# Kernel tuning notes

Measured on AMD Instinct MI355X. Metric: run time of the kernel, lower is better.

The kernel has to match this reference:

```python
import jax, jax.numpy as jnp
import numpy as np

HIDDEN = 512
HEADS = 8
NORM = 1.0 / np.sqrt(HIDDEN // HEADS)  # torch: 1/sqrt(tensor(dim_k)//head) = 1/8


def setup_inputs() -> dict:
    key = jax.random.key(0)
    ks = jax.random.split(key, 14)
    B, N, D = 2, 2048, HIDDEN
    s = 0.02
    d = {
        "x_re": jax.random.normal(ks[0], (B, N, D), dtype=jnp.float32),
        "x_im": jax.random.normal(ks[1], (B, N, D), dtype=jnp.float32),
    }
    names = ["Wq_re", "Wq_im", "bq_re", "bq_im",
             "Wk_re", "Wk_im", "bk_re", "bk_im",
             "Wv_re", "Wv_im", "bv_re", "bv_im"]
    for i, nm in enumerate(names):
        shape = (D, D) if nm.startswith("W") else (D,)
        d[nm] = jax.random.normal(ks[2 + i], shape, dtype=jnp.float32) * s
    return d


def reference(x_re, x_im,
              Wq_re, Wq_im, bq_re, bq_im,
              Wk_re, Wk_im, bk_re, bk_im,
              Wv_re, Wv_im, bv_re, bv_im):
    B, N, D = x_re.shape
    h, dk = HEADS, D // HEADS
    x = jax.lax.complex(x_re, x_im)
    Wq = jax.lax.complex(Wq_re, Wq_im); bq = jax.lax.complex(bq_re, bq_im)
    Wk = jax.lax.complex(Wk_re, Wk_im); bk = jax.lax.complex(bk_re, bk_im)
    Wv = jax.lax.complex(Wv_re, Wv_im); bv = jax.lax.complex(bv_re, bv_im)

    def proj(W, b):  # torch nn.Linear: x @ W.T + b, then split heads -> [B,h,N,dk]
        y = x @ W.T + b
        return y.reshape(B, N, h, dk).transpose(0, 2, 1, 3)

    q, k, v = proj(Wq, bq), proj(Wk, bk), proj(Wv, bv)
    # complex matmul (no conjugation, matching torch.matmul), scaled
    dist = jnp.einsum("bhnd,bhmd->bhnm", q, k) * NORM
    probs = jax.nn.softmax(jnp.abs(dist), axis=-1).astype(jnp.complex64)
    att = jnp.einsum("bhnm,bhmd->bhnd", probs, v)
    att = att.transpose(0, 2, 1, 3).reshape(B, N, D)
    # real-view output [B, N, D, 2]
    return jnp.stack([att.real, att.imag], axis=-1)
```

## Files before the change

### kernel.cpp

```cpp
#include <hip/hip_runtime.h>
#include <hip/hip_bf16.h>
#include <math.h>

#define B_ 2
#define N_ 2048
#define D_ 512
#define H_ 8
#define DK_ 64
#define M_ (B_ * N_)

typedef short s16x8 __attribute__((ext_vector_type(8)));
typedef short s16x4 __attribute__((ext_vector_type(4)));
typedef float fx4   __attribute__((ext_vector_type(4)));
typedef int   ix4   __attribute__((ext_vector_type(4)));

static __device__ __forceinline__ short f2bf(float f) {
    __hip_bfloat16 h = __float2bfloat16(f);
    return __builtin_bit_cast(short, h);
}
static __device__ __forceinline__ float bf2f(short s) {
    unsigned int u = ((unsigned int)(unsigned short)s) << 16;
    return __builtin_bit_cast(float, u);
}
static __device__ __forceinline__ float fexp2(float x) {
#if __has_builtin(__builtin_amdgcn_exp2f)
    return __builtin_amdgcn_exp2f(x);
#else
    return exp2f(x);
#endif
}
static __device__ __forceinline__ float fsqrt_(float x) {
#if __has_builtin(__builtin_amdgcn_sqrtf)
    return __builtin_amdgcn_sqrtf(x);
#else
    return sqrtf(x);
#endif
}
static __device__ __forceinline__ int pack_tr(float a, float b) {
    unsigned ua = __builtin_bit_cast(unsigned, a);
    unsigned ub = __builtin_bit_cast(unsigned, b);
    return (int)((ua >> 16) | (ub & 0xFFFF0000u));
}

#define MFMA16(a, b, c) __builtin_amdgcn_mfma_f32_16x16x32_bf16(a, b, c, 0, 0, 0)

#define C2_ 0.18033688f
#define M0_ 16.0f

__global__ __launch_bounds__(256, 2)
void qkproj_mfma(const float* __restrict__ xr, const float* __restrict__ xi,
                 const float* __restrict__ W0r, const float* __restrict__ W0i,
                 const float* __restrict__ b0r, const float* __restrict__ b0i,
                 const float* __restrict__ W1r, const float* __restrict__ W1i,
                 const float* __restrict__ b1r, const float* __restrict__ b1i,
                 short* __restrict__ o0r, short* __restrict__ o0i,
                 short* __restrict__ o1r, short* __restrict__ o1i)
{
    __shared__ short sA[2][128][40];
    __shared__ short sB[2][64][40];

    const int tid = threadIdx.x;
    const int w = tid >> 6, l = tid & 63, lg = l >> 4, lc = l & 15;
    const int wr = w >> 1, wc = w & 1;
    const int bn = blockIdx.x, bm = blockIdx.y, z = blockIdx.z;
    const float* Wr = z ? W1r : W0r;
    const float* Wi = z ? W1i : W0i;
    const float* br = z ? b1r : b0r;
    const float* bi = z ? b1i : b0i;
    short* outr = z ? o1r : o0r;
    short* outi = z ? o1i : o0i;

    const int srow = tid >> 3, scol = (tid & 7) * 4;
    int aoff = (bm * 128 + srow) * D_ + scol;
    int boff = (bn * 64 + srow) * D_ + scol;

    float4 rA[8], rB[4];
    auto issue = [&]() {
#pragma unroll
        for (int u = 0; u < 8; ++u) {
            const float* src = (u >= 4) ? xi : xr;
            rA[u] = *(const float4*)&src[aoff + (u & 3) * 32 * D_];
        }
#pragma unroll
        for (int u = 0; u < 4; ++u) {
            const float* src = (u >= 2) ? Wi : Wr;
            rB[u] = *(const float4*)&src[boff + (u & 1) * 32 * D_];
        }
        aoff += 32; boff += 32;
    };

    fx4 Cre[4][2], Cim[4][2];
#pragma unroll
    for (int mf = 0; mf < 4; ++mf)
#pragma unroll
        for (int nf = 0; nf < 2; ++nf)
#pragma unroll
            for (int j = 0; j < 4; ++j) { Cre[mf][nf][j] = 0.f; Cim[mf][nf][j] = 0.f; }

    issue();
    for (int k0 = 0; k0 < D_; k0 += 32) {
        __syncthreads();
#pragma unroll
        for (int u = 0; u < 8; ++u) {
            int comp = u >> 2, row = (u & 3) * 32 + srow;
            float vv[4] = {rA[u].x, rA[u].y, rA[u].z, rA[u].w};
            s16x4 hv;
#pragma unroll
            for (int q = 0; q < 4; ++q) hv[q] = f2bf(vv[q]);
            *(s16x4*)&sA[comp][row][scol] = hv;
        }
#pragma unroll
        for (int u = 0; u < 4; ++u) {
            int comp = u >> 1, row = (u & 1) * 32 + srow;
            float vv[4] = {rB[u].x, rB[u].y, rB[u].z, rB[u].w};
            s16x4 hv;
#pragma unroll
            for (int q = 0; q < 4; ++q) hv[q] = f2bf(vv[q]);
            *(s16x4*)&sB[comp][row][scol] = hv;
        }
        __syncthreads();
        if (k0 + 32 < D_) issue();

        s16x8 a[2][4];
#pragma unroll
        for (int comp = 0; comp < 2; ++comp)
#pragma unroll
            for (int mf = 0; mf < 4; ++mf)
                a[comp][mf] = *(const s16x8*)&sA[comp][wr * 64 + mf * 16 + lc][lg * 8];
        s16x8 bfr[2][2], bin[2];
#pragma unroll
        for (int comp = 0; comp < 2; ++comp)
#pragma unroll
            for (int nf = 0; nf < 2; ++nf)
                bfr[comp][nf] = *(const s16x8*)&sB[comp][wc * 32 + nf * 16 + lc][lg * 8];
#pragma unroll
        for (int nf = 0; nf < 2; ++nf) bin[nf] = bfr[1][nf] ^ (short)0x8000;

        __builtin_amdgcn_s_setprio(1);
#pragma unroll
        for (int mf = 0; mf < 4; ++mf)
#pragma unroll
            for (int nf = 0; nf < 2; ++nf) {
                Cre[mf][nf] = MFMA16(a[0][mf], bfr[0][nf], Cre[mf][nf]);
                Cre[mf][nf] = MFMA16(a[1][mf], bin[nf],    Cre[mf][nf]);
                Cim[mf][nf] = MFMA16(a[0][mf], bfr[1][nf], Cim[mf][nf]);
                Cim[mf][nf] = MFMA16(a[1][mf], bfr[0][nf], Cim[mf][nf]);
            }
        __builtin_amdgcn_s_setprio(0);
    }

    const int bb = (bm * 128) >> 11;
#pragma unroll
    for (int nf = 0; nf < 2; ++nf) {
        const int c = bn * 64 + wc * 32 + nf * 16 + lc;
        const float brv = br[c], biv = bi[c];
        const int h = c >> 6, dd = c & 63;
        const int n00 = (bm * 128 + wr * 64 + lg * 4) & (N_ - 1);
        size_t obase = (((size_t)(bb * H_ + h) * N_) + n00) * DK_ + dd;
#pragma unroll
        for (int mf = 0; mf < 4; ++mf)
#pragma unroll
            for (int j = 0; j < 4; ++j) {
                size_t o = obase + (size_t)(mf * 16 + j) * DK_;
                outr[o] = f2bf(Cre[mf][nf][j] + brv);
                outi[o] = f2bf(Cim[mf][nf][j] + biv);
            }
    }
}

__global__ __launch_bounds__(256, 2)
void vproj_mfma(const float* __restrict__ xr, const float* __restrict__ xi,
                const float* __restrict__ Wr, const float* __restrict__ Wi,
                const float* __restrict__ br, const float* __restrict__ bi,
                short* __restrict__ outr, short* __restrict__ outi)
{
    __shared__ short sA[2][2][64][40];
    __shared__ short sB[2][2][64][40];

    const int tid = threadIdx.x;
    const int w = tid >> 6, l = tid & 63, lg = l >> 4, lc = l & 15;
    const int wr = w >> 1, wc = w & 1;
    const int bn = blockIdx.x, bm = blockIdx.y;

    const int srow = tid >> 3, scol = (tid & 7) * 4;
    int aoff = (bm * 64 + srow) * D_ + scol;
    int boff = (bn * 64 + srow) * D_ + scol;

    float4 rA[4], rB[4];
    auto issue = [&]() {
#pragma unroll
        for (int u = 0; u < 4; ++u) {
            const float* src = (u >= 2) ? xi : xr;
            rA[u] = *(const float4*)&src[aoff + (u & 1) * 32 * D_];
        }
#pragma unroll
        for (int u = 0; u < 4; ++u) {
            const float* src = (u >= 2) ? Wi : Wr;
            rB[u] = *(const float4*)&src[boff + (u & 1) * 32 * D_];
        }
        aoff += 32; boff += 32;
    };

    fx4 Cre[2][2], Cim[2][2];
#pragma unroll
    for (int mf = 0; mf < 2; ++mf)
#pragma unroll
        for (int nf = 0; nf < 2; ++nf)
#pragma unroll
            for (int j = 0; j < 4; ++j) { Cre[mf][nf][j] = 0.f; Cim[mf][nf][j] = 0.f; }

    issue();
    for (int k0 = 0; k0 < D_; k0 += 32) {
        __syncthreads();
#pragma unroll
        for (int u = 0; u < 4; ++u) {
            int comp = u >> 1, row = (u & 1) * 32 + srow;
            float vv[4] = {rA[u].x, rA[u].y, rA[u].z, rA[u].w};
            s16x4 hv, lv;
#pragma unroll
            for (int q = 0; q < 4; ++q) {
                short hh = f2bf(vv[q]);
                hv[q] = hh;
                lv[q] = f2bf(vv[q] - bf2f(hh));
            }
            *(s16x4*)&sA[comp][0][row][scol] = hv;
            *(s16x4*)&sA[comp][1][row][scol] = lv;
        }
#pragma unroll
        for (int u = 0; u < 4; ++u) {
            int comp = u >> 1, row = (u & 1) * 32 + srow;
            float vv[4] = {rB[u].x, rB[u].y, rB[u].z, rB[u].w};
            s16x4 hv, lv;
#pragma unroll
            for (int q = 0; q < 4; ++q) {
                short hh = f2bf(vv[q]);
                hv[q] = hh;
                lv[q] = f2bf(vv[q] - bf2f(hh));
            }
            *(s16x4*)&sB[comp][0][row][scol] = hv;
            *(s16x4*)&sB[comp][1][row][scol] = lv;
        }
        __syncthreads();
        if (k0 + 32 < D_) issue();

        s16x8 a[2][2][2];
#pragma unroll
        for (int comp = 0; comp < 2; ++comp)
#pragma unroll
            for (int s = 0; s < 2; ++s)
#pragma unroll
                for (int mf = 0; mf < 2; ++mf)
                    a[comp][s][mf] = *(const s16x8*)&sA[comp][s][wr * 32 + mf * 16 + lc][lg * 8];
        s16x8 bfr[2][2][2], bin[2][2];
#pragma unroll
        for (int comp = 0; comp < 2; ++comp)
#pragma unroll
            for (int s = 0; s < 2; ++s)
#pragma unroll
                for (int nf = 0; nf < 2; ++nf)
                    bfr[comp][s][nf] = *(const s16x8*)&sB[comp][s][wc * 32 + nf * 16 + lc][lg * 8];
#pragma unroll
        for (int s = 0; s < 2; ++s)
#pragma unroll
            for (int nf = 0; nf < 2; ++nf)
                bin[s][nf] = bfr[1][s][nf] ^ (short)0x8000;

        __builtin_amdgcn_s_setprio(1);
#pragma unroll
        for (int mf = 0; mf < 2; ++mf)
#pragma unroll
            for (int nf = 0; nf < 2; ++nf) {
                fx4 cr = Cre[mf][nf], ci = Cim[mf][nf];
                cr = MFMA16(a[0][0][mf], bfr[0][0][nf], cr);
                cr = MFMA16(a[1][0][mf], bin[0][nf],    cr);
                ci = MFMA16(a[0][0][mf], bfr[1][0][nf], ci);
                ci = MFMA16(a[1][0][mf], bfr[0][0][nf], ci);
                cr = MFMA16(a[0][0][mf], bfr[0][1][nf], cr);
                cr = MFMA16(a[0][1][mf], bfr[0][0][nf], cr);
                cr = MFMA16(a[1][0][mf], bin[1][nf],    cr);
                cr = MFMA16(a[1][1][mf], bin[0][nf],    cr);
                ci = MFMA16(a[0][0][mf], bfr[1][1][nf], ci);
                ci = MFMA16(a[0][1][mf], bfr[1][0][nf], ci);
                ci = MFMA16(a[1][0][mf], bfr[0][1][nf], ci);
                ci = MFMA16(a[1][1][mf], bfr[0][0][nf], ci);
                Cre[mf][nf] = cr; Cim[mf][nf] = ci;
            }
        __builtin_amdgcn_s_setprio(0);
    }

    const int bb = (bm * 64) >> 11;
#pragma unroll
    for (int nf = 0; nf < 2; ++nf) {
        const int c = bn * 64 + wc * 32 + nf * 16 + lc;
        const float brv = br[c], biv = bi[c];
        const int h = c >> 6, dd = c & 63;
#pragma unroll
        for (int mf = 0; mf < 2; ++mf) {
            int m0 = bm * 64 + wr * 32 + mf * 16 + lg * 4;
            int n0 = m0 & (N_ - 1);
            s16x4 pr, pi;
#pragma unroll
            for (int j = 0; j < 4; ++j) {
                pr[j] = f2bf(Cre[mf][nf][j] + brv);
                pi[j] = f2bf(Cim[mf][nf][j] + biv);
            }
            size_t o = (((size_t)(bb * H_ + h) * DK_) + dd) * N_ + n0;
            *(s16x4*)&outr[o] = pr;
            *(s16x4*)&outi[o] = pi;
        }
    }
}

#define NT_ (N_ / 64)

__global__ __launch_bounds__(256, 2)
void attn_mfma(const short* __restrict__ qr, const short* __restrict__ qi,
               const short* __restrict__ kr, const short* __restrict__ ki,
               const short* __restrict__ vtr, const short* __restrict__ vti,
               float* __restrict__ out)
{
    __shared__ short sK [2][64][72];
    __shared__ short sVt[2][64][72];

    const int tid = threadIdx.x;
    const int w = tid >> 6, l = tid & 63, lg = l >> 4, lc = l & 15;

    const int dlin = blockIdx.y * 32 + blockIdx.x;
    const int xcd = dlin & 7, slot = dlin >> 3;
    const int bh = xcd * 2 + (slot >> 5);
    const int qt = slot & 31;
    const int b = bh >> 3, h = bh & 7;

    s16x8 Qr[2], Qi_[2], Qin[2];
    {
        size_t base = ((size_t)bh * N_ + (size_t)qt * 64 + w * 16 + lc) * DK_ + lg * 8;
        Qr[0]  = *(const s16x8*)&qr[base];
        Qr[1]  = *(const s16x8*)&qr[base + 32];
        Qi_[0] = *(const s16x8*)&qi[base];
        Qi_[1] = *(const s16x8*)&qi[base + 32];
        Qin[0] = Qi_[0] ^ (short)0x8000;
        Qin[1] = Qi_[1] ^ (short)0x8000;
    }

    s16x8 onesf;
#pragma unroll
    for (int u = 0; u < 8; ++u) onesf[u] = (short)0x3F80;

    fx4 o_re[4], o_im[4], o_l;
#pragma unroll
    for (int dt = 0; dt < 4; ++dt)
#pragma unroll
        for (int j = 0; j < 4; ++j) { o_re[dt][j] = 0.f; o_im[dt][j] = 0.f; }
#pragma unroll
    for (int j = 0; j < 4; ++j) o_l[j] = 0.f;

    const int rS = ((lc >> 2) << 3) | (lc & 3);

    const int srow = tid >> 3, scol8 = (tid & 7) * 8;
    int koff = bh * (N_ * DK_) + srow * DK_ + scol8;
    int voff = bh * (DK_ * N_) + srow * N_ + scol8;

    s16x8 rgK[4], rgV[4];
    auto issue = [&]() {
        rgK[0] = *(const s16x8*)&kr [koff];
        rgK[1] = *(const s16x8*)&kr [koff + 32 * DK_];
        rgK[2] = *(const s16x8*)&ki [koff];
        rgK[3] = *(const s16x8*)&ki [koff + 32 * DK_];
        rgV[0] = *(const s16x8*)&vtr[voff];
        rgV[1] = *(const s16x8*)&vtr[voff + 32 * N_];
        rgV[2] = *(const s16x8*)&vti[voff];
        rgV[3] = *(const s16x8*)&vti[voff + 32 * N_];
        koff += 64 * DK_; voff += 64;
    };

    issue();
    for (int kt = 0; kt < NT_; ++kt) {
        __syncthreads();
        *(s16x8*)&sK [0][srow     ][scol8] = rgK[0];
        *(s16x8*)&sK [0][srow + 32][scol8] = rgK[1];
        *(s16x8*)&sK [1][srow     ][scol8] = rgK[2];
        *(s16x8*)&sK [1][srow + 32][scol8] = rgK[3];
        *(s16x8*)&sVt[0][srow     ][scol8] = rgV[0];
        *(s16x8*)&sVt[0][srow + 32][scol8] = rgV[1];
        *(s16x8*)&sVt[1][srow     ][scol8] = rgV[2];
        *(s16x8*)&sVt[1][srow + 32][scol8] = rgV[3];
        __syncthreads();
        if (kt + 1 < NT_) issue();

        fx4 are[4], aim[4];
#pragma unroll
        for (int t = 0; t < 4; ++t)
#pragma unroll
            for (int j = 0; j < 4; ++j) { are[t][j] = 0.f; aim[t][j] = 0.f; }

        __builtin_amdgcn_s_setprio(1);
#pragma unroll
        for (int t = 0; t < 4; ++t) {
            const int row = rS + ((t & 1) << 2) + ((t >> 1) << 5);
#pragma unroll
            for (int c = 0; c < 2; ++c) {
                s16x8 Krf = *(const s16x8*)&sK[0][row][c * 32 + lg * 8];
                s16x8 Kif = *(const s16x8*)&sK[1][row][c * 32 + lg * 8];
                are[t] = MFMA16(Krf, Qr[c],  are[t]);
                are[t] = MFMA16(Kif, Qin[c], are[t]);
                aim[t] = MFMA16(Kif, Qr[c],  aim[t]);
                aim[t] = MFMA16(Krf, Qi_[c], aim[t]);
            }
        }
        __builtin_amdgcn_s_setprio(0);

        ix4 w0, w1;
#pragma unroll
        for (int t = 0; t < 4; ++t) {
            float p[4];
#pragma unroll
            for (int j = 0; j < 4; ++j) {
                float u2 = fmaf(are[t][j], are[t][j], aim[t][j] * aim[t][j]);
                p[j] = fexp2(fmaf(C2_, fsqrt_(u2), -M0_));
            }
            int d0 = pack_tr(p[0], p[1]);
            int d1 = pack_tr(p[2], p[3]);
            if (t == 0)      { w0[0] = d0; w0[1] = d1; }
            else if (t == 1) { w0[2] = d0; w0[3] = d1; }
            else if (t == 2) { w1[0] = d0; w1[1] = d1; }
            else             { w1[2] = d0; w1[3] = d1; }
        }
        s16x8 Pf0 = __builtin_bit_cast(s16x8, w0);
        s16x8 Pf1 = __builtin_bit_cast(s16x8, w1);

        __builtin_amdgcn_s_setprio(1);
        o_l = MFMA16(Pf0, onesf, o_l);
        o_l = MFMA16(Pf1, onesf, o_l);
#pragma unroll
        for (int dt = 0; dt < 4; ++dt) {
            s16x8 Vr0 = *(const s16x8*)&sVt[0][dt * 16 + lc][lg * 8];
            s16x8 Vi0 = *(const s16x8*)&sVt[1][dt * 16 + lc][lg * 8];
            o_re[dt] = MFMA16(Pf0, Vr0, o_re[dt]);
            o_im[dt] = MFMA16(Pf0, Vi0, o_im[dt]);
            s16x8 Vr1 = *(const s16x8*)&sVt[0][dt * 16 + lc][32 + lg * 8];
            s16x8 Vi1 = *(const s16x8*)&sVt[1][dt * 16 + lc][32 + lg * 8];
            o_re[dt] = MFMA16(Pf1, Vr1, o_re[dt]);
            o_im[dt] = MFMA16(Pf1, Vi1, o_im[dt]);
        }
        __builtin_amdgcn_s_setprio(0);
    }

    float inv[4];
#pragma unroll
    for (int j = 0; j < 4; ++j) inv[j] = 1.f / o_l[j];

    float2* po = (float2*)out;
#pragma unroll
    for (int dt = 0; dt < 4; ++dt)
#pragma unroll
        for (int j = 0; j < 4; ++j) {
            int n  = qt * 64 + w * 16 + lg * 4 + j;
            int dg = h * 64 + dt * 16 + lc;
            po[((size_t)b * N_ + n) * D_ + dg] =
                make_float2(o_re[dt][j] * inv[j], o_im[dt][j] * inv[j]);
        }
}

extern "C" void kernel_launch(void* const* d_in, const int* in_sizes, int n_in,
                              void* d_out, int out_size, void* d_ws, size_t ws_size,
                              hipStream_t stream)
{
    const float* xr = (const float*)d_in[0];
    const float* xi = (const float*)d_in[1];
    const float* Wq_r = (const float*)d_in[2];
    const float* Wq_i = (const float*)d_in[3];
    const float* bq_r = (const float*)d_in[4];
    const float* bq_i = (const float*)d_in[5];
    const float* Wk_r = (const float*)d_in[6];
    const float* Wk_i = (const float*)d_in[7];
    const float* bk_r = (const float*)d_in[8];
    const float* bk_i = (const float*)d_in[9];
    const float* Wv_r = (const float*)d_in[10];
    const float* Wv_i = (const float*)d_in[11];
    const float* bv_r = (const float*)d_in[12];
    const float* bv_i = (const float*)d_in[13];

    short* ws = (short*)d_ws;
    const size_t SZ = (size_t)B_ * H_ * N_ * DK_;
    short* qr_  = ws + 0 * SZ;
    short* qi_  = ws + 1 * SZ;
    short* kr_  = ws + 2 * SZ;
    short* ki_  = ws + 3 * SZ;
    short* vtr_ = ws + 4 * SZ;
    short* vti_ = ws + 5 * SZ;

    dim3 qkgrid(D_ / 64, M_ / 128, 2);
    qkproj_mfma<<<qkgrid, 256, 0, stream>>>(xr, xi,
                                            Wq_r, Wq_i, bq_r, bq_i,
                                            Wk_r, Wk_i, bk_r, bk_i,
                                            qr_, qi_, kr_, ki_);
    dim3 vgrid(D_ / 64, M_ / 64);
    vproj_mfma<<<vgrid, 256, 0, stream>>>(xr, xi, Wv_r, Wv_i, bv_r, bv_i, vtr_, vti_);

    dim3 agrid(N_ / 64, B_ * H_);
    attn_mfma<<<agrid, 256, 0, stream>>>(qr_, qi_, kr_, ki_, vtr_, vti_, (float*)d_out);
}
```

Baseline: 128.2 us.

## Double query tile per wave, double-buffer K/V in LDS with XOR-style swizzle

Each wave now handles 32 query rows instead of 16, so every K/V fragment loaded from LDS feeds twice as many MFMAs and the block covers 128 queries. The K/V shared tiles become double-buffered with a rotating swizzle instead of padding, which drops one barrier per iteration and aims to avoid LDS bank conflicts. The grid halves to 256 blocks with launch bounds lowered to one block per SIMD set. This trades more registers and fewer resident blocks for less LDS and global K/V traffic per query.

```diff
diff --git a/kernel.cpp b/kernel.cpp
--- a/kernel.cpp
+++ b/kernel.cpp
@@ -313,52 +313,63 @@
 
 #define NT_ (N_ / 64)
 
-__global__ __launch_bounds__(256, 2)
+static __device__ __forceinline__ int swz8(int row, int slot) {
+    return (slot + (row & 7) + 2 * ((row >> 3) & 3)) & 7;
+}
+
+__global__ __launch_bounds__(256, 1)
 void attn_mfma(const short* __restrict__ qr, const short* __restrict__ qi,
                const short* __restrict__ kr, const short* __restrict__ ki,
                const short* __restrict__ vtr, const short* __restrict__ vti,
                float* __restrict__ out)
 {
-    __shared__ short sK [2][64][72];
-    __shared__ short sVt[2][64][72];
+    __shared__ short sK [2][2][64][64];
+    __shared__ short sVt[2][2][64][64];
 
     const int tid = threadIdx.x;
     const int w = tid >> 6, l = tid & 63, lg = l >> 4, lc = l & 15;
 
-    const int dlin = blockIdx.y * 32 + blockIdx.x;
+    const int dlin = blockIdx.y * 16 + blockIdx.x;
     const int xcd = dlin & 7, slot = dlin >> 3;
-    const int bh = xcd * 2 + (slot >> 5);
-    const int qt = slot & 31;
+    const int bh = xcd * 2 + (slot >> 4);
+    const int qt = slot & 15;
     const int b = bh >> 3, h = bh & 7;
 
-    s16x8 Qr[2], Qi_[2], Qin[2];
-    {
-        size_t base = ((size_t)bh * N_ + (size_t)qt * 64 + w * 16 + lc) * DK_ + lg * 8;
-        Qr[0]  = *(const s16x8*)&qr[base];
-        Qr[1]  = *(const s16x8*)&qr[base + 32];
-        Qi_[0] = *(const s16x8*)&qi[base];
-        Qi_[1] = *(const s16x8*)&qi[base + 32];
-        Qin[0] = Qi_[0] ^ (short)0x8000;
-        Qin[1] = Qi_[1] ^ (short)0x8000;
+    s16x8 Qr[2][2], Qi_[2][2], Qin[2][2];
+#pragma unroll
+    for (int qh = 0; qh < 2; ++qh) {
+        size_t base = ((size_t)bh * N_ + (size_t)qt * 128 + w * 32 + qh * 16 + lc) * DK_ + lg * 8;
+#pragma unroll
+        for (int c = 0; c < 2; ++c) {
+            Qr[qh][c]  = *(const s16x8*)&qr[base + c * 32];
+            Qi_[qh][c] = *(const s16x8*)&qi[base + c * 32];
+            Qin[qh][c] = Qi_[qh][c] ^ (short)0x8000;
+        }
     }
 
     s16x8 onesf;
 #pragma unroll
     for (int u = 0; u < 8; ++u) onesf[u] = (short)0x3F80;
 
-    fx4 o_re[4], o_im[4], o_l;
-#pragma unroll
-    for (int dt = 0; dt < 4; ++dt)
-#pragma unroll
-        for (int j = 0; j < 4; ++j) { o_re[dt][j] = 0.f; o_im[dt][j] = 0.f; }
-#pragma unroll
-    for (int j = 0; j < 4; ++j) o_l[j] = 0.f;
+    fx4 o_re[2][4], o_im[2][4], o_l[2];
+#pragma unroll
+    for (int qh = 0; qh < 2; ++qh) {
+#pragma unroll
+        for (int dt = 0; dt < 4; ++dt)
+#pragma unroll
+            for (int j = 0; j < 4; ++j) { o_re[qh][dt][j] = 0.f; o_im[qh][dt][j] = 0.f; }
+#pragma unroll
+        for (int j = 0; j < 4; ++j) o_l[qh][j] = 0.f;
+    }
 
     const int rS = ((lc >> 2) << 3) | (lc & 3);
-
-    const int srow = tid >> 3, scol8 = (tid & 7) * 8;
-    int koff = bh * (N_ * DK_) + srow * DK_ + scol8;
-    int voff = bh * (DK_ * N_) + srow * N_ + scol8;
+    const int bqs = lg + (lc & 3) + 2 * (lc >> 2);
+    const int bvs = lg + (lc & 7) + 2 * (lc >> 3);
+
+    const int srow = tid >> 3, cs = tid & 7;
+    const int sw = swz8(srow, cs) * 8;
+    int koff = bh * (N_ * DK_) + srow * DK_ + cs * 8;
+    int voff = bh * (DK_ * N_) + srow * N_ + cs * 8;
 
     s16x8 rgK[4], rgV[4];
     auto issue = [&]() {
@@ -372,26 +383,31 @@
         rgV[3] = *(const s16x8*)&vti[voff + 32 * N_];
         koff += 64 * DK_; voff += 64;
     };
+    auto stage = [&](int bi) {
+        *(s16x8*)&sK [bi][0][srow     ][sw] = rgK[0];
+        *(s16x8*)&sK [bi][0][srow + 32][sw] = rgK[1];
+        *(s16x8*)&sK [bi][1][srow     ][sw] = rgK[2];
+        *(s16x8*)&sK [bi][1][srow + 32][sw] = rgK[3];
+        *(s16x8*)&sVt[bi][0][srow     ][sw] = rgV[0];
+        *(s16x8*)&sVt[bi][0][srow + 32][sw] = rgV[1];
+        *(s16x8*)&sVt[bi][1][srow     ][sw] = rgV[2];
+        *(s16x8*)&sVt[bi][1][srow + 32][sw] = rgV[3];
+    };
 
     issue();
+    stage(0);
     for (int kt = 0; kt < NT_; ++kt) {
-        __syncthreads();
-        *(s16x8*)&sK [0][srow     ][scol8] = rgK[0];
-        *(s16x8*)&sK [0][srow + 32][scol8] = rgK[1];
-        *(s16x8*)&sK [1][srow     ][scol8] = rgK[2];
-        *(s16x8*)&sK [1][srow + 32][scol8] = rgK[3];
-        *(s16x8*)&sVt[0][srow     ][scol8] = rgV[0];
-        *(s16x8*)&sVt[0][srow + 32][scol8] = rgV[1];
-        *(s16x8*)&sVt[1][srow     ][scol8] = rgV[2];
-        *(s16x8*)&sVt[1][srow + 32][scol8] = rgV[3];
+        const int bi = kt & 1;
         __syncthreads();
         if (kt + 1 < NT_) issue();
 
-        fx4 are[4], aim[4];
-#pragma unroll
-        for (int t = 0; t < 4; ++t)
-#pragma unroll
-            for (int j = 0; j < 4; ++j) { are[t][j] = 0.f; aim[t][j] = 0.f; }
+        fx4 are[2][4], aim[2][4];
+#pragma unroll
+        for (int qh = 0; qh < 2; ++qh)
+#pragma unroll
+            for (int t = 0; t < 4; ++t)
+#pragma unroll
+                for (int j = 0; j < 4; ++j) { are[qh][t][j] = 0.f; aim[qh][t][j] = 0.f; }
 
         __builtin_amdgcn_s_setprio(1);
 #pragma unroll
@@ -399,66 +415,87 @@
             const int row = rS + ((t & 1) << 2) + ((t >> 1) << 5);
 #pragma unroll
             for (int c = 0; c < 2; ++c) {
-                s16x8 Krf = *(const s16x8*)&sK[0][row][c * 32 + lg * 8];
-                s16x8 Kif = *(const s16x8*)&sK[1][row][c * 32 + lg * 8];
-                are[t] = MFMA16(Krf, Qr[c],  are[t]);
-                are[t] = MFMA16(Kif, Qin[c], are[t]);
-                aim[t] = MFMA16(Kif, Qr[c],  aim[t]);
-                aim[t] = MFMA16(Krf, Qi_[c], aim[t]);
+                const int sl = ((bqs + 4 * ((c + t) & 1)) & 7) * 8;
+                s16x8 Krf = *(const s16x8*)&sK[bi][0][row][sl];
+                s16x8 Kif = *(const s16x8*)&sK[bi][1][row][sl];
+#pragma unroll
+                for (int qh = 0; qh < 2; ++qh) {
+                    are[qh][t] = MFMA16(Krf, Qr[qh][c],  are[qh][t]);
+                    are[qh][t] = MFMA16(Kif, Qin[qh][c], are[qh][t]);
+                    aim[qh][t] = MFMA16(Kif, Qr[qh][c],  aim[qh][t]);
+                    aim[qh][t] = MFMA16(Krf, Qi_[qh][c], aim[qh][t]);
+                }
             }
         }
         __builtin_amdgcn_s_setprio(0);
 
-        ix4 w0, w1;
-#pragma unroll
-        for (int t = 0; t < 4; ++t) {
-            float p[4];
+        s16x8 Pf[2][2];
+#pragma unroll
+        for (int qh = 0; qh < 2; ++qh) {
+            ix4 w0, w1;
+#pragma unroll
+            for (int t = 0; t < 4; ++t) {
+                float p[4];
+#pragma unroll
+                for (int j = 0; j < 4; ++j) {
+                    float u2 = fmaf(are[qh][t][j], are[qh][t][j], aim[qh][t][j] * aim[qh][t][j]);
+                    p[j] = fexp2(fmaf(C2_, fsqrt_(u2), -M0_));
+                }
+                int d0 = pack_tr(p[0], p[1]);
+                int d1 = pack_tr(p[2], p[3]);
+                if (t == 0)      { w0[0] = d0; w0[1] = d1; }
+                else if (t == 1) { w0[2] = d0; w0[3] = d1; }
+                else if (t == 2) { w1[0] = d0; w1[1] = d1; }
+                else             { w1[2] = d0; w1[3] = d1; }
+            }
+            Pf[qh][0] = __builtin_bit_cast(s16x8, w0);
+            Pf[qh][1] = __builtin_bit_cast(s16x8, w1);
+        }
+
+        __builtin_amdgcn_s_setprio(1);
+#pragma unroll
+        for (int qh = 0; qh < 2; ++qh) {
+            o_l[qh] = MFMA16(Pf[qh][0], onesf, o_l[qh]);
+            o_l[qh] = MFMA16(Pf[qh][1], onesf, o_l[qh]);
+        }
+#pragma unroll
+        for (int dt = 0; dt < 4; ++dt) {
+            const int d = dt * 16 + lc;
+            const int s0 = ((bvs + 4 * dt) & 7) * 8;
+            const int s1 = ((bvs + 4 * dt + 4) & 7) * 8;
+            s16x8 Vr0 = *(const s16x8*)&sVt[bi][0][d][s0];
+            s16x8 Vi0 = *(const s16x8*)&sVt[bi][1][d][s0];
+            s16x8 Vr1 = *(const s16x8*)&sVt[bi][0][d][s1];
+            s16x8 Vi1 = *(const s16x8*)&sVt[bi][1][d][s1];
+#pragma unroll
+            for (int qh = 0; qh < 2; ++qh) {
+                o_re[qh][dt] = MFMA16(Pf[qh][0], Vr0, o_re[qh][dt]);
+                o_im[qh][dt] = MFMA16(Pf[qh][0], Vi0, o_im[qh][dt]);
+                o_re[qh][dt] = MFMA16(Pf[qh][1], Vr1, o_re[qh][dt]);
+                o_im[qh][dt] = MFMA16(Pf[qh][1], Vi1, o_im[qh][dt]);
+            }
+        }
+        __builtin_amdgcn_s_setprio(0);
+
+        if (kt + 1 < NT_) stage((kt + 1) & 1);
+    }
+
+    float2* po = (float2*)out;
+#pragma unroll
+    for (int qh = 0; qh < 2; ++qh) {
+        float inv[4];
+#pragma unroll
+        for (int j = 0; j < 4; ++j) inv[j] = 1.f / o_l[qh][j];
+#pragma unroll
+        for (int dt = 0; dt < 4; ++dt)
 #pragma unroll
             for (int j = 0; j < 4; ++j) {
-                float u2 = fmaf(are[t][j], are[t][j], aim[t][j] * aim[t][j]);
-                p[j] = fexp2(fmaf(C2_, fsqrt_(u2), -M0_));
-            }
-            int d0 = pack_tr(p[0], p[1]);
-            int d1 = pack_tr(p[2], p[3]);
-            if (t == 0)      { w0[0] = d0; w0[1] = d1; }
-            else if (t == 1) { w0[2] = d0; w0[3] = d1; }
-            else if (t == 2) { w1[0] = d0; w1[1] = d1; }
-            else             { w1[2] = d0; w1[3] = d1; }
-        }
-        s16x8 Pf0 = __builtin_bit_cast(s16x8, w0);
-        s16x8 Pf1 = __builtin_bit_cast(s16x8, w1);
-
-        __builtin_amdgcn_s_setprio(1);
-        o_l = MFMA16(Pf0, onesf, o_l);
-        o_l = MFMA16(Pf1, onesf, o_l);
-#pragma unroll
-        for (int dt = 0; dt < 4; ++dt) {
-            s16x8 Vr0 = *(const s16x8*)&sVt[0][dt * 16 + lc][lg * 8];
-            s16x8 Vi0 = *(const s16x8*)&sVt[1][dt * 16 + lc][lg * 8];
-            o_re[dt] = MFMA16(Pf0, Vr0, o_re[dt]);
-            o_im[dt] = MFMA16(Pf0, Vi0, o_im[dt]);
-            s16x8 Vr1 = *(const s16x8*)&sVt[0][dt * 16 + lc][32 + lg * 8];
-            s16x8 Vi1 = *(const s16x8*)&sVt[1][dt * 16 + lc][32 + lg * 8];
-            o_re[dt] = MFMA16(Pf1, Vr1, o_re[dt]);
-            o_im[dt] = MFMA16(Pf1, Vi1, o_im[dt]);
-        }
-        __builtin_amdgcn_s_setprio(0);
-    }
-
-    float inv[4];
-#pragma unroll
-    for (int j = 0; j < 4; ++j) inv[j] = 1.f / o_l[j];
-
-    float2* po = (float2*)out;
-#pragma unroll
-    for (int dt = 0; dt < 4; ++dt)
-#pragma unroll
-        for (int j = 0; j < 4; ++j) {
-            int n  = qt * 64 + w * 16 + lg * 4 + j;
-            int dg = h * 64 + dt * 16 + lc;
-            po[((size_t)b * N_ + n) * D_ + dg] =
-                make_float2(o_re[dt][j] * inv[j], o_im[dt][j] * inv[j]);
-        }
+                int n  = qt * 128 + w * 32 + qh * 16 + lg * 4 + j;
+                int dg = h * 64 + dt * 16 + lc;
+                po[((size_t)b * N_ + n) * D_ + dg] =
+                    make_float2(o_re[qh][dt][j] * inv[j], o_im[qh][dt][j] * inv[j]);
+            }
+    }
 }
 
 extern "C" void kernel_launch(void* const* d_in, const int* in_sizes, int n_in,
@@ -497,6 +534,6 @@
     dim3 vgrid(D_ / 64, M_ / 64);
     vproj_mfma<<<vgrid, 256, 0, stream>>>(xr, xi, Wv_r, Wv_i, bv_r, bv_i, vtr_, vti_);
 
-    dim3 agrid(N_ / 64, B_ * H_);
+    dim3 agrid(16, 16);
     attn_mfma<<<agrid, 256, 0, stream>>>(qr_, qi_, kr_, ki_, vtr_, vti_, (float*)d_out);
 }
```

After: 136.9 us. 6.7% more time.
